# Kernel tuning notes

Hardware: AMD Instinct MI355X
Metric: run time of the kernel (lower is better)

The kernel has to match this reference:

```python
import jax, jax.numpy as jnp
import numpy as np

N_NODES = 100000
N_EDGES = 1600000
F_IN = 64
HID = 128
N_CLASSES = 16
N_GRAPHS = 128


def _glorot(key, shape):
    fan_in = shape[1]
    bound = 1.0 / np.sqrt(fan_in)
    return jax.random.uniform(key, shape, jnp.float32, -bound, bound)


def setup_inputs() -> dict:
    key = jax.random.key(0)
    ks = jax.random.split(key, 12)
    x = jax.random.normal(ks[0], (N_NODES, F_IN), jnp.float32)
    edge_index = jax.random.randint(ks[1], (2, N_EDGES), 0, N_NODES, jnp.int64)
    batch = jnp.sort(jax.random.randint(ks[2], (N_NODES,), 0, N_GRAPHS, jnp.int64))
    # GraphConv l: out = lin_rel(sum_j x_j) + lin_root(x); lin_rel has bias, lin_root does not.
    W1_rel = _glorot(ks[3], (HID, F_IN)); b1 = jnp.zeros((HID,), jnp.float32)
    W1_root = _glorot(ks[4], (HID, F_IN))
    W2_rel = _glorot(ks[5], (HID, HID)); b2 = jnp.zeros((HID,), jnp.float32)
    W2_root = _glorot(ks[6], (HID, HID))
    W3_rel = _glorot(ks[7], (HID, HID)); b3 = jnp.zeros((HID,), jnp.float32)
    W3_root = _glorot(ks[8], (HID, HID))
    W_lin = _glorot(ks[9], (N_CLASSES, HID))
    b_lin = jnp.zeros((N_CLASSES,), jnp.float32)
    return {"x": x, "edge_index": edge_index, "batch": batch,
            "W1_rel": W1_rel, "b1": b1, "W1_root": W1_root,
            "W2_rel": W2_rel, "b2": b2, "W2_root": W2_root,
            "W3_rel": W3_rel, "b3": b3, "W3_root": W3_root,
            "W_lin": W_lin, "b_lin": b_lin}


def graph_conv(x, src, dst, W_rel, b_rel, W_root):
    # gather messages from source nodes, scatter-add at targets
    agg = jax.ops.segment_sum(x[src], dst, num_segments=N_NODES)  # [N, in]
    return agg @ W_rel.T + b_rel + x @ W_root.T


def reference(x, edge_index, batch, W1_rel, b1, W1_root, W2_rel, b2, W2_root,
              W3_rel, b3, W3_root, W_lin, b_lin):
    src, dst = edge_index[0], edge_index[1]
    h = jax.nn.relu(graph_conv(x, src, dst, W1_rel, b1, W1_root))
    h = jax.nn.relu(graph_conv(h, src, dst, W2_rel, b2, W2_root))
    h = graph_conv(h, src, dst, W3_rel, b3, W3_root)
    # global_mean_pool over batch ids
    sums = jax.ops.segment_sum(h, batch, num_segments=N_GRAPHS)  # [G, HID]
    counts = jax.ops.segment_sum(jnp.ones((h.shape[0],), h.dtype), batch,
                                 num_segments=N_GRAPHS)
    pooled = sums / jnp.maximum(counts, 1.0)[:, None]
    # dropout is identity in eval mode
    return pooled @ W_lin.T + b_lin
```

## Files before the change

### kernel.cpp

```cpp
#include <hip/hip_runtime.h>

#define N_NODES_C 100000
#define N_GRAPHS_C 128

typedef __attribute__((ext_vector_type(8))) __bf16 bf16x8;
typedef __attribute__((ext_vector_type(4))) float f32x4;

__device__ __forceinline__ f32x4 mfma16(bf16x8 a, bf16x8 b, f32x4 c) {
    return __builtin_amdgcn_mfma_f32_16x16x32_bf16(a, b, c, 0, 0, 0);
}

__global__ void hist_kernel(const int* __restrict__ ei, int E, int* __restrict__ deg) {
    int i = blockIdx.x * blockDim.x + threadIdx.x;
    if (i < E) atomicAdd(&deg[ei[E + i]], 1);
}

__global__ void scan1_kernel(const int* __restrict__ deg, int N,
                             int* __restrict__ tmp, int* __restrict__ bsum) {
    __shared__ int sh[512];
    int t = threadIdx.x;
    int i = blockIdx.x * 512 + t;
    int v = (i < N) ? deg[i] : 0;
    sh[t] = v;
    __syncthreads();
    for (int off = 1; off < 512; off <<= 1) {
        int add = (t >= off) ? sh[t - off] : 0;
        __syncthreads();
        sh[t] += add;
        __syncthreads();
    }
    if (i < N) tmp[i] = sh[t] - v;
    if (t == 511) bsum[blockIdx.x] = sh[511];
}

__global__ void scan2_kernel(int* bsum, int nb) {
    if (threadIdx.x == 0 && blockIdx.x == 0) {
        int run = 0;
        for (int j = 0; j < nb; ++j) { int v = bsum[j]; bsum[j] = run; run += v; }
    }
}

__global__ void scan3_kernel(const int* __restrict__ tmp, const int* __restrict__ bsum,
                             int N, int* __restrict__ rowp, int* __restrict__ rowpm) {
    int i = blockIdx.x * 512 + threadIdx.x;
    if (i < N) {
        int v = tmp[i] + bsum[blockIdx.x];
        rowp[i] = v;
        rowpm[i] = v;
    }
}

#define FILL_EPT 8
__global__ void fill_kernel(const int* __restrict__ ei, int E,
                            int* __restrict__ rowpm, int* __restrict__ csr) {
    int p = blockIdx.y;
    int base = blockIdx.x * 256 * FILL_EPT + threadIdx.x;
#pragma unroll
    for (int k = 0; k < FILL_EPT; ++k) {
        int i = base + k * 256;
        if (i < E) {
            int d = ei[E + i];
            if ((d >> 13) == p) {
                int pos = atomicAdd(&rowpm[d], 1);
                csr[pos] = ei[i];
            }
        }
    }
}

template <int FIN>
__global__ __launch_bounds__(256) void agg_kernel(const float* __restrict__ xin,
                                                  const int* __restrict__ rowp,
                                                  const int* __restrict__ degv,
                                                  const int* __restrict__ csrc,
                                                  float* __restrict__ aggout, int nNodes) {
    int wave = blockIdx.x * 4 + (threadIdx.x >> 6);
    int lane = threadIdx.x & 63;
    if (wave >= nNodes) return;
    int start = rowp[wave];
    int deg = degv[wave];
    const float4* x4 = (const float4*)xin;
    constexpr int EPW = (FIN == 128) ? 2 : 4;
    constexpr int RS = FIN / 4;
    const int grp = lane / RS;
    const int f4 = lane & (RS - 1);

    float4 acc[8];
#pragma unroll
    for (int q = 0; q < 8; ++q) acc[q] = make_float4(0.f, 0.f, 0.f, 0.f);

    for (int base = 0; base < deg; base += 64) {
        int cnt = min(64, deg - base);
        int sid = (lane < cnt) ? csrc[start + base + lane] : 0;
        int j = 0;
        for (; j + 8 * EPW <= cnt; j += 8 * EPW) {
            int n[8];
#pragma unroll
            for (int q = 0; q < 8; ++q) n[q] = __shfl(sid, j + q * EPW + grp);
            float4 v[8];
#pragma unroll
            for (int q = 0; q < 8; ++q) v[q] = x4[(size_t)n[q] * RS + f4];
#pragma unroll
            for (int q = 0; q < 8; ++q) {
                acc[q].x += v[q].x; acc[q].y += v[q].y;
                acc[q].z += v[q].z; acc[q].w += v[q].w;
            }
        }
        for (; j + EPW <= cnt; j += EPW) {
            int n0 = __shfl(sid, j + grp);
            float4 v = x4[(size_t)n0 * RS + f4];
            acc[0].x += v.x; acc[0].y += v.y; acc[0].z += v.z; acc[0].w += v.w;
        }
        for (; j < cnt; ++j) {
            int n0 = __shfl(sid, j);
            if (grp == 0) {
                float4 v = x4[(size_t)n0 * RS + f4];
                acc[0].x += v.x; acc[0].y += v.y; acc[0].z += v.z; acc[0].w += v.w;
            }
        }
    }
    float4 tot;
    tot.x = ((acc[0].x+acc[1].x)+(acc[2].x+acc[3].x)) + ((acc[4].x+acc[5].x)+(acc[6].x+acc[7].x));
    tot.y = ((acc[0].y+acc[1].y)+(acc[2].y+acc[3].y)) + ((acc[4].y+acc[5].y)+(acc[6].y+acc[7].y));
    tot.z = ((acc[0].z+acc[1].z)+(acc[2].z+acc[3].z)) + ((acc[4].z+acc[5].z)+(acc[6].z+acc[7].z));
    tot.w = ((acc[0].w+acc[1].w)+(acc[2].w+acc[3].w)) + ((acc[4].w+acc[5].w)+(acc[6].w+acc[7].w));
    if (FIN == 64) {
        tot.x += __shfl_xor(tot.x, 16); tot.y += __shfl_xor(tot.y, 16);
        tot.z += __shfl_xor(tot.z, 16); tot.w += __shfl_xor(tot.w, 16);
    }
    tot.x += __shfl_xor(tot.x, 32); tot.y += __shfl_xor(tot.y, 32);
    tot.z += __shfl_xor(tot.z, 32); tot.w += __shfl_xor(tot.w, 32);
    if (lane < RS)
        ((float4*)aggout)[(size_t)wave * RS + lane] = tot;
}

__global__ void wprep_kernel(const float* __restrict__ Wrel, const float* __restrict__ Wroot,
                             int KH, unsigned* __restrict__ img) {
    int cid = blockIdx.x;
    int col = threadIdx.x;
    int key = (col >> 1) & 3;
    unsigned hiw[16], low[16];
#pragma unroll 4
    for (int p = 0; p < 16; ++p) {
        int k0 = cid * 32 + p * 2;
        float v0 = (k0 < KH) ? Wrel[col * KH + k0] : Wroot[col * KH + k0 - KH];
        float v1 = (k0 + 1 < KH) ? Wrel[col * KH + k0 + 1] : Wroot[col * KH + k0 + 1 - KH];
        unsigned u0 = __float_as_uint(v0), u1 = __float_as_uint(v1);
        unsigned h0 = u0 & 0xFFFF0000u, h1 = u1 & 0xFFFF0000u;
        float l0 = v0 - __uint_as_float(h0), l1 = v1 - __uint_as_float(h1);
        unsigned lb0 = __float_as_uint(l0) & 0xFFFF0000u;
        unsigned lb1 = __float_as_uint(l1) & 0xFFFF0000u;
        hiw[p] = (h0 >> 16) | h1;
        low[p] = (lb0 >> 16) | lb1;
    }
    unsigned* cb = img + (size_t)cid * 4096;
#pragma unroll 4
    for (int p = 0; p < 16; ++p) {
        int s = p >> 2, w = p & 3;
        int sp = s ^ key;
        cb[col * 16 + sp * 4 + w] = hiw[p];
        cb[2048 + col * 16 + sp * 4 + w] = low[p];
    }
}

template <int KTOT, bool RELU>
__global__ __launch_bounds__(256, 2) void xform_kernel(
    const float* __restrict__ agg, const float* __restrict__ xin,
    const unsigned* __restrict__ wimg, const float* __restrict__ bias,
    float* __restrict__ hout, int nNodes)
{
    constexpr int KH = KTOT / 2;
    constexpr int NC = KTOT / 32;
    __shared__ unsigned sA[2][4096];
    __shared__ unsigned sW[2][4096];
    const int t = threadIdx.x;
    const int nb0 = blockIdx.x * 128;

    const int srow = t >> 1;
    const int skh = t & 1;
    const int skey = (srow >> 1) & 3;
    const int gn = nb0 + srow;
    const bool gvalid = gn < nNodes;
    const size_t arow = (size_t)gn * KH;

    float4 va[4]; uint4 vw[4];
    auto loadChunk = [&](int cix) {
        int kc = cix * 32 + skh * 16;
        const float* srcA = (kc < KH) ? agg : xin;
        int kof = (kc < KH) ? kc : kc - KH;
        if (gvalid) {
#pragma unroll
            for (int q = 0; q < 4; ++q)
                va[q] = *(const float4*)&srcA[arow + kof + q * 4];
        } else {
#pragma unroll
            for (int q = 0; q < 4; ++q) va[q] = make_float4(0.f, 0.f, 0.f, 0.f);
        }
        const uint4* wsrc = (const uint4*)(wimg + (size_t)cix * 4096) + t * 4;
#pragma unroll
        for (int q = 0; q < 4; ++q) vw[q] = wsrc[q];
    };
    auto writeChunk = [&](int buf) {
        uint4* wd = (uint4*)&sW[buf][t * 16];
#pragma unroll
        for (int q = 0; q < 4; ++q) wd[q] = vw[q];
        unsigned hiw[8], low[8];
#pragma unroll
        for (int q = 0; q < 4; ++q) {
            float vv[4] = {va[q].x, va[q].y, va[q].z, va[q].w};
#pragma unroll
            for (int h = 0; h < 2; ++h) {
                unsigned u0 = __float_as_uint(vv[h * 2]), u1 = __float_as_uint(vv[h * 2 + 1]);
                unsigned h0 = u0 & 0xFFFF0000u, h1 = u1 & 0xFFFF0000u;
                float l0 = vv[h * 2] - __uint_as_float(h0);
                float l1 = vv[h * 2 + 1] - __uint_as_float(h1);
                unsigned lb0 = __float_as_uint(l0) & 0xFFFF0000u;
                unsigned lb1 = __float_as_uint(l1) & 0xFFFF0000u;
                hiw[q * 2 + h] = (h0 >> 16) | h1;
                low[q * 2 + h] = (lb0 >> 16) | lb1;
            }
        }
        int s0 = (skh * 2) ^ skey, s1 = (skh * 2 + 1) ^ skey;
        unsigned* abH = &sA[buf][srow * 16];
        unsigned* abL = &sA[buf][2048 + srow * 16];
        *(uint4*)&abH[s0 * 4] = make_uint4(hiw[0], hiw[1], hiw[2], hiw[3]);
        *(uint4*)&abH[s1 * 4] = make_uint4(hiw[4], hiw[5], hiw[6], hiw[7]);
        *(uint4*)&abL[s0 * 4] = make_uint4(low[0], low[1], low[2], low[3]);
        *(uint4*)&abL[s1 * 4] = make_uint4(low[4], low[5], low[6], low[7]);
    };

    const int lane = t & 63, wv = t >> 6;
    const int r15 = lane & 15, hi4 = lane >> 4;
    const int ckey = (r15 >> 1) & 3;
    const int cslot = (hi4 ^ ckey) * 4;
    const int arow0 = (wv * 32 + r15) * 16;
    const int arow1 = arow0 + 256;

    f32x4 acc[2][8];
#pragma unroll
    for (int g = 0; g < 2; ++g)
#pragma unroll
        for (int j = 0; j < 8; ++j) acc[g][j] = (f32x4){0.f, 0.f, 0.f, 0.f};

    float bj[8];
#pragma unroll
    for (int j = 0; j < 8; ++j) bj[j] = bias[j * 16 + r15];

    loadChunk(0);
    writeChunk(0);
    if (NC > 1) loadChunk(1);
    __syncthreads();

#pragma unroll 1
    for (int cix = 0; cix < NC; ++cix) {
        const int cur = cix & 1;
        if (cix + 1 < NC) {
            writeChunk(cur ^ 1);
            if (cix + 2 < NC) loadChunk(cix + 2);
        }
        const unsigned* A = sA[cur];
        const unsigned* W = sW[cur];
        bf16x8 ah0 = *(const bf16x8*)&A[arow0 + cslot];
        bf16x8 ah1 = *(const bf16x8*)&A[arow1 + cslot];
        bf16x8 al0 = *(const bf16x8*)&A[2048 + arow0 + cslot];
        bf16x8 al1 = *(const bf16x8*)&A[2048 + arow1 + cslot];
#pragma unroll
        for (int j = 0; j < 8; ++j) {
            int cb = (j * 16 + r15) * 16;
            bf16x8 bh = *(const bf16x8*)&W[cb + cslot];
            bf16x8 bl = *(const bf16x8*)&W[2048 + cb + cslot];
            acc[0][j] = mfma16(ah0, bh, acc[0][j]);
            acc[1][j] = mfma16(ah1, bh, acc[1][j]);
            acc[0][j] = mfma16(ah0, bl, acc[0][j]);
            acc[1][j] = mfma16(ah1, bl, acc[1][j]);
            acc[0][j] = mfma16(al0, bh, acc[0][j]);
            acc[1][j] = mfma16(al1, bh, acc[1][j]);
        }
        __syncthreads();
    }

#pragma unroll
    for (int g2 = 0; g2 < 2; ++g2) {
#pragma unroll
        for (int r = 0; r < 4; ++r) {
            int node = nb0 + wv * 32 + g2 * 16 + hi4 * 4 + r;
            if (node >= nNodes) continue;
            float* orow = &hout[(size_t)node * 128];
#pragma unroll
            for (int j = 0; j < 8; ++j) {
                float v = acc[g2][j][r] + bj[j];
                if (RELU) v = fmaxf(v, 0.f);
                orow[j * 16 + r15] = v;
            }
        }
    }
}

__global__ void bounds_kernel(const int* __restrict__ batch, int N, int* __restrict__ gstart) {
    int g = blockIdx.x * blockDim.x + threadIdx.x;
    if (g > N_GRAPHS_C) return;
    int lo = 0, hi = N;
    while (lo < hi) {
        int mid = (lo + hi) >> 1;
        if (batch[mid] < g) lo = mid + 1; else hi = mid;
    }
    gstart[g] = lo;
}

__global__ __launch_bounds__(256) void pool2_kernel(const float* __restrict__ h,
                                                    const int* __restrict__ gstart,
                                                    float* __restrict__ pooled) {
    int g = blockIdx.x;
    int f4 = threadIdx.x & 31;
    int sub = threadIdx.x >> 5;
    int s = gstart[g], e = gstart[g + 1];
    const float4* h4 = (const float4*)h;
    float4 acc = make_float4(0.f, 0.f, 0.f, 0.f);
    for (int n = s + sub; n < e; n += 8) {
        float4 v = h4[(size_t)n * 32 + f4];
        acc.x += v.x; acc.y += v.y; acc.z += v.z; acc.w += v.w;
    }
    __shared__ float4 sh[8][33];
    sh[sub][f4] = acc;
    __syncthreads();
    if (sub == 0) {
        float4 tot = acc;
#pragma unroll
        for (int q = 1; q < 8; ++q) {
            float4 v = sh[q][f4];
            tot.x += v.x; tot.y += v.y; tot.z += v.z; tot.w += v.w;
        }
        float inv = 1.0f / fmaxf((float)(e - s), 1.0f);
        tot.x *= inv; tot.y *= inv; tot.z *= inv; tot.w *= inv;
        ((float4*)pooled)[g * 32 + f4] = tot;
    }
}

__global__ void final_kernel(const float* __restrict__ pooled,
                             const float* __restrict__ Wlin, const float* __restrict__ blin,
                             float* __restrict__ out) {
    int idx = blockIdx.x * blockDim.x + threadIdx.x;
    int g = idx >> 4, c = idx & 15;
    float s = 0.f;
    for (int k = 0; k < 128; ++k) s += pooled[g * 128 + k] * Wlin[c * 128 + k];
    out[idx] = s + blin[c];
}

extern "C" void kernel_launch(void* const* d_in, const int* in_sizes, int n_in,
                              void* d_out, int out_size, void* d_ws, size_t ws_size,
                              hipStream_t stream) {
    const float* x      = (const float*)d_in[0];
    const int*   ei     = (const int*)d_in[1];
    const int*   batch  = (const int*)d_in[2];
    const float* W1_rel = (const float*)d_in[3];
    const float* b1     = (const float*)d_in[4];
    const float* W1_root= (const float*)d_in[5];
    const float* W2_rel = (const float*)d_in[6];
    const float* b2     = (const float*)d_in[7];
    const float* W2_root= (const float*)d_in[8];
    const float* W3_rel = (const float*)d_in[9];
    const float* b3     = (const float*)d_in[10];
    const float* W3_root= (const float*)d_in[11];
    const float* W_lin  = (const float*)d_in[12];
    const float* b_lin  = (const float*)d_in[13];
    float* out = (float*)d_out;

    const int N = in_sizes[2];
    const int E = in_sizes[1] / 2;
    const int nb = (N + 511) / 512;

    char* base = (char*)d_ws;
    size_t off = 0;
    auto carve = [&](size_t bytes) -> void* {
        void* p = base + off;
        off = (off + bytes + 255) & ~(size_t)255;
        return p;
    };
    int*      deg    = (int*)carve((size_t)N * 4);
    int*      tmp    = (int*)carve((size_t)N * 4);
    int*      bsum   = (int*)carve(1024);
    int*      rowp   = (int*)carve((size_t)(N + 1) * 4);
    int*      rowpm  = (int*)carve((size_t)N * 4);
    int*      csr    = (int*)carve((size_t)E * 4);
    float*    aggbuf = (float*)carve((size_t)N * 128 * 4);
    float*    hA     = (float*)carve((size_t)N * 128 * 4);
    float*    hB     = (float*)carve((size_t)N * 128 * 4);
    float*    pooled = (float*)carve((size_t)N_GRAPHS_C * 128 * 4);
    int*      gstart = (int*)carve((size_t)(N_GRAPHS_C + 1) * 4);
    unsigned* wimg1  = (unsigned*)carve((size_t)4 * 4096 * 4);
    unsigned* wimg2  = (unsigned*)carve((size_t)8 * 4096 * 4);
    unsigned* wimg3  = (unsigned*)carve((size_t)8 * 4096 * 4);
    (void)ws_size;

    hipMemsetAsync(deg, 0, (size_t)N * 4, stream);

    wprep_kernel<<<4, 128, 0, stream>>>(W1_rel, W1_root, 64, wimg1);
    wprep_kernel<<<8, 128, 0, stream>>>(W2_rel, W2_root, 128, wimg2);
    wprep_kernel<<<8, 128, 0, stream>>>(W3_rel, W3_root, 128, wimg3);

    hist_kernel<<<(E + 255) / 256, 256, 0, stream>>>(ei, E, deg);
    scan1_kernel<<<nb, 512, 0, stream>>>(deg, N, tmp, bsum);
    scan2_kernel<<<1, 64, 0, stream>>>(bsum, nb);
    scan3_kernel<<<nb, 512, 0, stream>>>(tmp, bsum, N, rowp, rowpm);
    const int npass = (N + 8191) >> 13;
    fill_kernel<<<dim3((E + 256 * FILL_EPT - 1) / (256 * FILL_EPT), npass), 256, 0, stream>>>(
        ei, E, rowpm, csr);

    bounds_kernel<<<1, 192, 0, stream>>>(batch, N, gstart);

    const int aggGrid = (N + 3) / 4;
    const int xGrid = (N + 127) / 128;

    agg_kernel<64><<<aggGrid, 256, 0, stream>>>(x, rowp, deg, csr, aggbuf, N);
    xform_kernel<128, true><<<xGrid, 256, 0, stream>>>(aggbuf, x, wimg1, b1, hA, N);

    agg_kernel<128><<<aggGrid, 256, 0, stream>>>(hA, rowp, deg, csr, aggbuf, N);
    xform_kernel<256, true><<<xGrid, 256, 0, stream>>>(aggbuf, hA, wimg2, b2, hB, N);

    agg_kernel<128><<<aggGrid, 256, 0, stream>>>(hB, rowp, deg, csr, aggbuf, N);
    xform_kernel<256, false><<<xGrid, 256, 0, stream>>>(aggbuf, hB, wimg3, b3, hA, N);

    pool2_kernel<<<N_GRAPHS_C, 256, 0, stream>>>(hA, gstart, pooled);
    final_kernel<<<8, 256, 0, stream>>>(pooled, W_lin, b_lin, out);
}
```

Before: 789.0 us.

## Fuse neighbor aggregation into the MFMA transform kernel per GraphConv layer

```diff
diff --git a/kernel.cpp b/kernel.cpp
--- a/kernel.cpp
+++ b/kernel.cpp
@@ -8,6 +8,16 @@
 
 __device__ __forceinline__ f32x4 mfma16(bf16x8 a, bf16x8 b, f32x4 c) {
     return __builtin_amdgcn_mfma_f32_16x16x32_bf16(a, b, c, 0, 0, 0);
+}
+
+__device__ __forceinline__ void split2(float a, float b, unsigned& hi, unsigned& lo) {
+    unsigned ua = __float_as_uint(a), ub = __float_as_uint(b);
+    unsigned ha = ua & 0xFFFF0000u, hb = ub & 0xFFFF0000u;
+    float la = a - __uint_as_float(ha), lb = b - __uint_as_float(hb);
+    unsigned lpa = __float_as_uint(la) & 0xFFFF0000u;
+    unsigned lpb = __float_as_uint(lb) & 0xFFFF0000u;
+    hi = (ha >> 16) | hb;
+    lo = (lpa >> 16) | lpb;
 }
 
 __global__ void hist_kernel(const int* __restrict__ ei, int E, int* __restrict__ deg) {
@@ -68,72 +78,6 @@
     }
 }
 
-template <int FIN>
-__global__ __launch_bounds__(256) void agg_kernel(const float* __restrict__ xin,
-                                                  const int* __restrict__ rowp,
-                                                  const int* __restrict__ degv,
-                                                  const int* __restrict__ csrc,
-                                                  float* __restrict__ aggout, int nNodes) {
-    int wave = blockIdx.x * 4 + (threadIdx.x >> 6);
-    int lane = threadIdx.x & 63;
-    if (wave >= nNodes) return;
-    int start = rowp[wave];
-    int deg = degv[wave];
-    const float4* x4 = (const float4*)xin;
-    constexpr int EPW = (FIN == 128) ? 2 : 4;
-    constexpr int RS = FIN / 4;
-    const int grp = lane / RS;
-    const int f4 = lane & (RS - 1);
-
-    float4 acc[8];
-#pragma unroll
-    for (int q = 0; q < 8; ++q) acc[q] = make_float4(0.f, 0.f, 0.f, 0.f);
-
-    for (int base = 0; base < deg; base += 64) {
-        int cnt = min(64, deg - base);
-        int sid = (lane < cnt) ? csrc[start + base + lane] : 0;
-        int j = 0;
-        for (; j + 8 * EPW <= cnt; j += 8 * EPW) {
-            int n[8];
-#pragma unroll
-            for (int q = 0; q < 8; ++q) n[q] = __shfl(sid, j + q * EPW + grp);
-            float4 v[8];
-#pragma unroll
-            for (int q = 0; q < 8; ++q) v[q] = x4[(size_t)n[q] * RS + f4];
-#pragma unroll
-            for (int q = 0; q < 8; ++q) {
-                acc[q].x += v[q].x; acc[q].y += v[q].y;
-                acc[q].z += v[q].z; acc[q].w += v[q].w;
-            }
-        }
-        for (; j + EPW <= cnt; j += EPW) {
-            int n0 = __shfl(sid, j + grp);
-            float4 v = x4[(size_t)n0 * RS + f4];
-            acc[0].x += v.x; acc[0].y += v.y; acc[0].z += v.z; acc[0].w += v.w;
-        }
-        for (; j < cnt; ++j) {
-            int n0 = __shfl(sid, j);
-            if (grp == 0) {
-                float4 v = x4[(size_t)n0 * RS + f4];
-                acc[0].x += v.x; acc[0].y += v.y; acc[0].z += v.z; acc[0].w += v.w;
-            }
-        }
-    }
-    float4 tot;
-    tot.x = ((acc[0].x+acc[1].x)+(acc[2].x+acc[3].x)) + ((acc[4].x+acc[5].x)+(acc[6].x+acc[7].x));
-    tot.y = ((acc[0].y+acc[1].y)+(acc[2].y+acc[3].y)) + ((acc[4].y+acc[5].y)+(acc[6].y+acc[7].y));
-    tot.z = ((acc[0].z+acc[1].z)+(acc[2].z+acc[3].z)) + ((acc[4].z+acc[5].z)+(acc[6].z+acc[7].z));
-    tot.w = ((acc[0].w+acc[1].w)+(acc[2].w+acc[3].w)) + ((acc[4].w+acc[5].w)+(acc[6].w+acc[7].w));
-    if (FIN == 64) {
-        tot.x += __shfl_xor(tot.x, 16); tot.y += __shfl_xor(tot.y, 16);
-        tot.z += __shfl_xor(tot.z, 16); tot.w += __shfl_xor(tot.w, 16);
-    }
-    tot.x += __shfl_xor(tot.x, 32); tot.y += __shfl_xor(tot.y, 32);
-    tot.z += __shfl_xor(tot.z, 32); tot.w += __shfl_xor(tot.w, 32);
-    if (lane < RS)
-        ((float4*)aggout)[(size_t)wave * RS + lane] = tot;
-}
-
 __global__ void wprep_kernel(const float* __restrict__ Wrel, const float* __restrict__ Wroot,
                              int KH, unsigned* __restrict__ img) {
     int cid = blockIdx.x;
@@ -145,13 +89,7 @@
         int k0 = cid * 32 + p * 2;
         float v0 = (k0 < KH) ? Wrel[col * KH + k0] : Wroot[col * KH + k0 - KH];
         float v1 = (k0 + 1 < KH) ? Wrel[col * KH + k0 + 1] : Wroot[col * KH + k0 + 1 - KH];
-        unsigned u0 = __float_as_uint(v0), u1 = __float_as_uint(v1);
-        unsigned h0 = u0 & 0xFFFF0000u, h1 = u1 & 0xFFFF0000u;
-        float l0 = v0 - __uint_as_float(h0), l1 = v1 - __uint_as_float(h1);
-        unsigned lb0 = __float_as_uint(l0) & 0xFFFF0000u;
-        unsigned lb1 = __float_as_uint(l1) & 0xFFFF0000u;
-        hiw[p] = (h0 >> 16) | h1;
-        low[p] = (lb0 >> 16) | lb1;
+        split2(v0, v1, hiw[p], low[p]);
     }
     unsigned* cb = img + (size_t)cid * 4096;
 #pragma unroll 4
@@ -163,135 +101,189 @@
     }
 }
 
-template <int KTOT, bool RELU>
-__global__ __launch_bounds__(256, 2) void xform_kernel(
-    const float* __restrict__ agg, const float* __restrict__ xin,
+template <int KH, bool RELU>
+__global__ __launch_bounds__(256, 2) void fused_kernel(
+    const float* __restrict__ xin,
+    const int* __restrict__ rowp, const int* __restrict__ degv,
+    const int* __restrict__ csrc,
     const unsigned* __restrict__ wimg, const float* __restrict__ bias,
     float* __restrict__ hout, int nNodes)
 {
-    constexpr int KH = KTOT / 2;
-    constexpr int NC = KTOT / 32;
-    __shared__ unsigned sA[2][4096];
+    constexpr int NC  = (2 * KH) / 32;
+    constexpr int NCA = KH / 32;
+    constexpr int RS  = KH / 4;
+    constexpr int EPW = 64 / RS;
+    __shared__ unsigned sAgg[NCA * 2048];
     __shared__ unsigned sW[2][4096];
+    __shared__ unsigned sX[2][2048];
     const int t = threadIdx.x;
-    const int nb0 = blockIdx.x * 128;
-
-    const int srow = t >> 1;
-    const int skh = t & 1;
+    const int nb0 = blockIdx.x * 64;
+    const int lane = t & 63, wv = t >> 6;
+
+    uint4 vw[4];
+    {
+        const uint4* ws = (const uint4*)wimg + t * 4;
+#pragma unroll
+        for (int q = 0; q < 4; ++q) vw[q] = ws[q];
+    }
+
+    {
+        const float4* x4 = (const float4*)xin;
+        const int grp = lane / RS;
+        const int f4 = lane & (RS - 1);
+        for (int ni = 0; ni < 16; ++ni) {
+            const int node = nb0 + wv * 16 + ni;
+            float4 a[8];
+#pragma unroll
+            for (int q = 0; q < 8; ++q) a[q] = make_float4(0.f, 0.f, 0.f, 0.f);
+            if (node < nNodes) {
+                int start = rowp[node], deg = degv[node];
+                for (int base = 0; base < deg; base += 64) {
+                    int cnt = min(64, deg - base);
+                    int sid = (lane < cnt) ? csrc[start + base + lane] : 0;
+                    int j = 0;
+                    for (; j + 8 * EPW <= cnt; j += 8 * EPW) {
+                        int n[8];
+#pragma unroll
+                        for (int q = 0; q < 8; ++q) n[q] = __shfl(sid, j + q * EPW + grp);
+                        float4 v[8];
+#pragma unroll
+                        for (int q = 0; q < 8; ++q) v[q] = x4[(size_t)n[q] * RS + f4];
+#pragma unroll
+                        for (int q = 0; q < 8; ++q) {
+                            a[q].x += v[q].x; a[q].y += v[q].y;
+                            a[q].z += v[q].z; a[q].w += v[q].w;
+                        }
+                    }
+                    for (; j + EPW <= cnt; j += EPW) {
+                        int n0 = __shfl(sid, j + grp);
+                        float4 v = x4[(size_t)n0 * RS + f4];
+                        a[0].x += v.x; a[0].y += v.y; a[0].z += v.z; a[0].w += v.w;
+                    }
+                    for (; j < cnt; ++j) {
+                        int n0 = __shfl(sid, j);
+                        if (grp == 0) {
+                            float4 v = x4[(size_t)n0 * RS + f4];
+                            a[0].x += v.x; a[0].y += v.y; a[0].z += v.z; a[0].w += v.w;
+                        }
+                    }
+                }
+            }
+            float4 tot;
+            tot.x = ((a[0].x+a[1].x)+(a[2].x+a[3].x)) + ((a[4].x+a[5].x)+(a[6].x+a[7].x));
+            tot.y = ((a[0].y+a[1].y)+(a[2].y+a[3].y)) + ((a[4].y+a[5].y)+(a[6].y+a[7].y));
+            tot.z = ((a[0].z+a[1].z)+(a[2].z+a[3].z)) + ((a[4].z+a[5].z)+(a[6].z+a[7].z));
+            tot.w = ((a[0].w+a[1].w)+(a[2].w+a[3].w)) + ((a[4].w+a[5].w)+(a[6].w+a[7].w));
+            if (RS == 16) {
+                tot.x += __shfl_xor(tot.x, 16); tot.y += __shfl_xor(tot.y, 16);
+                tot.z += __shfl_xor(tot.z, 16); tot.w += __shfl_xor(tot.w, 16);
+            }
+            tot.x += __shfl_xor(tot.x, 32); tot.y += __shfl_xor(tot.y, 32);
+            tot.z += __shfl_xor(tot.z, 32); tot.w += __shfl_xor(tot.w, 32);
+            if (grp < 2) {
+                unsigned h0, l0, h1, l1;
+                split2(tot.x, tot.y, h0, l0);
+                split2(tot.z, tot.w, h1, l1);
+                int row = wv * 16 + ni;
+                int key = (row >> 1) & 3;
+                int c = f4 >> 3;
+                int u = (2 * f4) & 15;
+                int sp = (u >> 2) ^ key;
+                unsigned* dst = &sAgg[c * 2048 + grp * 1024 + row * 16 + sp * 4 + (u & 3)];
+                dst[0] = (grp == 0) ? h0 : l0;
+                dst[1] = (grp == 0) ? h1 : l1;
+            }
+        }
+    }
+
+    const int srow = t >> 2;
+    const int kq = t & 3;
     const int skey = (srow >> 1) & 3;
-    const int gn = nb0 + srow;
-    const bool gvalid = gn < nNodes;
-    const size_t arow = (size_t)gn * KH;
-
-    float4 va[4]; uint4 vw[4];
-    auto loadChunk = [&](int cix) {
-        int kc = cix * 32 + skh * 16;
-        const float* srcA = (kc < KH) ? agg : xin;
-        int kof = (kc < KH) ? kc : kc - KH;
-        if (gvalid) {
-#pragma unroll
-            for (int q = 0; q < 4; ++q)
-                va[q] = *(const float4*)&srcA[arow + kof + q * 4];
+    const bool svalid = (nb0 + srow) < nNodes;
+    float4 vx0, vx1;
+    auto loadW = [&](int cix) {
+        const uint4* ws = (const uint4*)(wimg + (size_t)cix * 4096) + t * 4;
+#pragma unroll
+        for (int q = 0; q < 4; ++q) vw[q] = ws[q];
+    };
+    auto loadX = [&](int cix) {
+        int kofs = (cix - NCA) * 32 + kq * 8;
+        if (svalid) {
+            const float* p = &xin[(size_t)(nb0 + srow) * KH + kofs];
+            vx0 = *(const float4*)p;
+            vx1 = *(const float4*)(p + 4);
         } else {
-#pragma unroll
-            for (int q = 0; q < 4; ++q) va[q] = make_float4(0.f, 0.f, 0.f, 0.f);
-        }
-        const uint4* wsrc = (const uint4*)(wimg + (size_t)cix * 4096) + t * 4;
-#pragma unroll
-        for (int q = 0; q < 4; ++q) vw[q] = wsrc[q];
+            vx0 = make_float4(0.f, 0.f, 0.f, 0.f);
+            vx1 = vx0;
+        }
     };
-    auto writeChunk = [&](int buf) {
+    auto writeW = [&](int buf) {
         uint4* wd = (uint4*)&sW[buf][t * 16];
 #pragma unroll
         for (int q = 0; q < 4; ++q) wd[q] = vw[q];
-        unsigned hiw[8], low[8];
-#pragma unroll
-        for (int q = 0; q < 4; ++q) {
-            float vv[4] = {va[q].x, va[q].y, va[q].z, va[q].w};
-#pragma unroll
-            for (int h = 0; h < 2; ++h) {
-                unsigned u0 = __float_as_uint(vv[h * 2]), u1 = __float_as_uint(vv[h * 2 + 1]);
-                unsigned h0 = u0 & 0xFFFF0000u, h1 = u1 & 0xFFFF0000u;
-                float l0 = vv[h * 2] - __uint_as_float(h0);
-                float l1 = vv[h * 2 + 1] - __uint_as_float(h1);
-                unsigned lb0 = __float_as_uint(l0) & 0xFFFF0000u;
-                unsigned lb1 = __float_as_uint(l1) & 0xFFFF0000u;
-                hiw[q * 2 + h] = (h0 >> 16) | h1;
-                low[q * 2 + h] = (lb0 >> 16) | lb1;
-            }
-        }
-        int s0 = (skh * 2) ^ skey, s1 = (skh * 2 + 1) ^ skey;
-        unsigned* abH = &sA[buf][srow * 16];
-        unsigned* abL = &sA[buf][2048 + srow * 16];
-        *(uint4*)&abH[s0 * 4] = make_uint4(hiw[0], hiw[1], hiw[2], hiw[3]);
-        *(uint4*)&abH[s1 * 4] = make_uint4(hiw[4], hiw[5], hiw[6], hiw[7]);
-        *(uint4*)&abL[s0 * 4] = make_uint4(low[0], low[1], low[2], low[3]);
-        *(uint4*)&abL[s1 * 4] = make_uint4(low[4], low[5], low[6], low[7]);
     };
-
-    const int lane = t & 63, wv = t >> 6;
+    auto writeX = [&](int buf) {
+        unsigned h[4], l[4];
+        split2(vx0.x, vx0.y, h[0], l[0]); split2(vx0.z, vx0.w, h[1], l[1]);
+        split2(vx1.x, vx1.y, h[2], l[2]); split2(vx1.z, vx1.w, h[3], l[3]);
+        int sp = (kq ^ skey) * 4;
+        *(uint4*)&sX[buf][srow * 16 + sp] = make_uint4(h[0], h[1], h[2], h[3]);
+        *(uint4*)&sX[buf][1024 + srow * 16 + sp] = make_uint4(l[0], l[1], l[2], l[3]);
+    };
+
     const int r15 = lane & 15, hi4 = lane >> 4;
     const int ckey = (r15 >> 1) & 3;
     const int cslot = (hi4 ^ ckey) * 4;
-    const int arow0 = (wv * 32 + r15) * 16;
-    const int arow1 = arow0 + 256;
-
-    f32x4 acc[2][8];
-#pragma unroll
-    for (int g = 0; g < 2; ++g)
-#pragma unroll
-        for (int j = 0; j < 8; ++j) acc[g][j] = (f32x4){0.f, 0.f, 0.f, 0.f};
-
+    const int arow = (wv * 16 + r15) * 16;
+
+    f32x4 acc[8];
+#pragma unroll
+    for (int j = 0; j < 8; ++j) acc[j] = (f32x4){0.f, 0.f, 0.f, 0.f};
     float bj[8];
 #pragma unroll
     for (int j = 0; j < 8; ++j) bj[j] = bias[j * 16 + r15];
 
-    loadChunk(0);
-    writeChunk(0);
-    if (NC > 1) loadChunk(1);
+    writeW(0);
+    if (NC > 1) { loadW(1); if (1 >= NCA) loadX(1); }
     __syncthreads();
 
 #pragma unroll 1
     for (int cix = 0; cix < NC; ++cix) {
         const int cur = cix & 1;
         if (cix + 1 < NC) {
-            writeChunk(cur ^ 1);
-            if (cix + 2 < NC) loadChunk(cix + 2);
-        }
-        const unsigned* A = sA[cur];
+            writeW(cur ^ 1);
+            if (cix + 1 >= NCA) writeX(cur ^ 1);
+            if (cix + 2 < NC) {
+                loadW(cix + 2);
+                if (cix + 2 >= NCA) loadX(cix + 2);
+            }
+        }
+        const unsigned* Ah = (cix < NCA) ? &sAgg[cix * 2048] : &sX[cur][0];
         const unsigned* W = sW[cur];
-        bf16x8 ah0 = *(const bf16x8*)&A[arow0 + cslot];
-        bf16x8 ah1 = *(const bf16x8*)&A[arow1 + cslot];
-        bf16x8 al0 = *(const bf16x8*)&A[2048 + arow0 + cslot];
-        bf16x8 al1 = *(const bf16x8*)&A[2048 + arow1 + cslot];
+        bf16x8 ah = *(const bf16x8*)&Ah[arow + cslot];
+        bf16x8 al = *(const bf16x8*)&Ah[1024 + arow + cslot];
 #pragma unroll
         for (int j = 0; j < 8; ++j) {
             int cb = (j * 16 + r15) * 16;
             bf16x8 bh = *(const bf16x8*)&W[cb + cslot];
             bf16x8 bl = *(const bf16x8*)&W[2048 + cb + cslot];
-            acc[0][j] = mfma16(ah0, bh, acc[0][j]);
-            acc[1][j] = mfma16(ah1, bh, acc[1][j]);
-            acc[0][j] = mfma16(ah0, bl, acc[0][j]);
-            acc[1][j] = mfma16(ah1, bl, acc[1][j]);
-            acc[0][j] = mfma16(al0, bh, acc[0][j]);
-            acc[1][j] = mfma16(al1, bh, acc[1][j]);
+            acc[j] = mfma16(ah, bh, acc[j]);
+            acc[j] = mfma16(ah, bl, acc[j]);
+            acc[j] = mfma16(al, bh, acc[j]);
         }
         __syncthreads();
     }
 
 #pragma unroll
-    for (int g2 = 0; g2 < 2; ++g2) {
-#pragma unroll
-        for (int r = 0; r < 4; ++r) {
-            int node = nb0 + wv * 32 + g2 * 16 + hi4 * 4 + r;
-            if (node >= nNodes) continue;
-            float* orow = &hout[(size_t)node * 128];
-#pragma unroll
-            for (int j = 0; j < 8; ++j) {
-                float v = acc[g2][j][r] + bj[j];
-                if (RELU) v = fmaxf(v, 0.f);
-                orow[j * 16 + r15] = v;
-            }
+    for (int r = 0; r < 4; ++r) {
+        int node = nb0 + wv * 16 + hi4 * 4 + r;
+        if (node >= nNodes) continue;
+        float* orow = &hout[(size_t)node * 128];
+#pragma unroll
+        for (int j = 0; j < 8; ++j) {
+            float v = acc[j][r] + bj[j];
+            if (RELU) v = fmaxf(v, 0.f);
+            orow[j * 16 + r15] = v;
         }
     }
 }
@@ -382,7 +374,6 @@
     int*      rowp   = (int*)carve((size_t)(N + 1) * 4);
     int*      rowpm  = (int*)carve((size_t)N * 4);
     int*      csr    = (int*)carve((size_t)E * 4);
-    float*    aggbuf = (float*)carve((size_t)N * 128 * 4);
     float*    hA     = (float*)carve((size_t)N * 128 * 4);
     float*    hB     = (float*)carve((size_t)N * 128 * 4);
     float*    pooled = (float*)carve((size_t)N_GRAPHS_C * 128 * 4);
@@ -408,17 +399,16 @@
 
     bounds_kernel<<<1, 192, 0, stream>>>(batch, N, gstart);
 
-    const int aggGrid = (N + 3) / 4;
-    const int xGrid = (N + 127) / 128;
-
-    agg_kernel<64><<<aggGrid, 256, 0, stream>>>(x, rowp, deg, csr, aggbuf, N);
-    xform_kernel<128, true><<<xGrid, 256, 0, stream>>>(aggbuf, x, wimg1, b1, hA, N);
-
-    agg_kernel<128><<<aggGrid, 256, 0, stream>>>(hA, rowp, deg, csr, aggbuf, N);
-    xform_kernel<256, true><<<xGrid, 256, 0, stream>>>(aggbuf, hA, wimg2, b2, hB, N);
-
-    agg_kernel<128><<<aggGrid, 256, 0, stream>>>(hB, rowp, deg, csr, aggbuf, N);
-    xform_kernel<256, false><<<xGrid, 256, 0, stream>>>(aggbuf, hB, wimg3, b3, hA, N);
+    const int fGrid = (N + 63) / 64;
+
+    fused_kernel<64, true><<<fGrid, 256, 0, stream>>>(
+        x, rowp, deg, csr, wimg1, b1, hA, N);
+
+    fused_kernel<128, true><<<fGrid, 256, 0, stream>>>(
+        hA, rowp, deg, csr, wimg2, b2, hB, N);
+
+    fused_kernel<128, false><<<fGrid, 256, 0, stream>>>(
+        hB, rowp, deg, csr, wimg3, b3, hA, N);
 
     pool2_kernel<<<N_GRAPHS_C, 256, 0, stream>>>(hA, gstart, pooled);
     final_kernel<<<8, 256, 0, stream>>>(pooled, W_lin, b_lin, out);
```

New measurement: 1.079 ms. +36.7%, slower.

## Load MFMA fragments directly from global memory, bypassing LDS staging in xform

Applied to the files above, without the earlier changes.

```diff
diff --git a/kernel.cpp b/kernel.cpp
--- a/kernel.cpp
+++ b/kernel.cpp
@@ -8,6 +8,25 @@
 
 __device__ __forceinline__ f32x4 mfma16(bf16x8 a, bf16x8 b, f32x4 c) {
     return __builtin_amdgcn_mfma_f32_16x16x32_bf16(a, b, c, 0, 0, 0);
+}
+
+__device__ __forceinline__ void split2(float a, float b, unsigned& hi, unsigned& lo) {
+    unsigned ua = __float_as_uint(a), ub = __float_as_uint(b);
+    unsigned ha = ua & 0xFFFF0000u, hb = ub & 0xFFFF0000u;
+    float la = a - __uint_as_float(ha), lb = b - __uint_as_float(hb);
+    unsigned lpa = __float_as_uint(la) & 0xFFFF0000u;
+    unsigned lpb = __float_as_uint(lb) & 0xFFFF0000u;
+    hi = (ha >> 16) | hb;
+    lo = (lpa >> 16) | lpb;
+}
+
+__device__ __forceinline__ void splitfrag(float4 v0, float4 v1, bf16x8& hi, bf16x8& lo) {
+    unsigned h[4], l[4];
+    split2(v0.x, v0.y, h[0], l[0]); split2(v0.z, v0.w, h[1], l[1]);
+    split2(v1.x, v1.y, h[2], l[2]); split2(v1.z, v1.w, h[3], l[3]);
+    uint4 uh = make_uint4(h[0], h[1], h[2], h[3]);
+    uint4 ul = make_uint4(l[0], l[1], l[2], l[3]);
+    hi = *(bf16x8*)&uh; lo = *(bf16x8*)&ul;
 }
 
 __global__ void hist_kernel(const int* __restrict__ ei, int E, int* __restrict__ deg) {
@@ -136,139 +155,68 @@
 
 __global__ void wprep_kernel(const float* __restrict__ Wrel, const float* __restrict__ Wroot,
                              int KH, unsigned* __restrict__ img) {
-    int cid = blockIdx.x;
-    int col = threadIdx.x;
-    int key = (col >> 1) & 3;
-    unsigned hiw[16], low[16];
-#pragma unroll 4
-    for (int p = 0; p < 16; ++p) {
-        int k0 = cid * 32 + p * 2;
-        float v0 = (k0 < KH) ? Wrel[col * KH + k0] : Wroot[col * KH + k0 - KH];
-        float v1 = (k0 + 1 < KH) ? Wrel[col * KH + k0 + 1] : Wroot[col * KH + k0 + 1 - KH];
-        unsigned u0 = __float_as_uint(v0), u1 = __float_as_uint(v1);
-        unsigned h0 = u0 & 0xFFFF0000u, h1 = u1 & 0xFFFF0000u;
-        float l0 = v0 - __uint_as_float(h0), l1 = v1 - __uint_as_float(h1);
-        unsigned lb0 = __float_as_uint(l0) & 0xFFFF0000u;
-        unsigned lb1 = __float_as_uint(l1) & 0xFFFF0000u;
-        hiw[p] = (h0 >> 16) | h1;
-        low[p] = (lb0 >> 16) | lb1;
-    }
-    unsigned* cb = img + (size_t)cid * 4096;
-#pragma unroll 4
-    for (int p = 0; p < 16; ++p) {
-        int s = p >> 2, w = p & 3;
-        int sp = s ^ key;
-        cb[col * 16 + sp * 4 + w] = hiw[p];
-        cb[2048 + col * 16 + sp * 4 + w] = low[p];
-    }
+    int cj = blockIdx.x;
+    int l = threadIdx.x;
+    int c = cj >> 3, j = cj & 7;
+    int col = j * 16 + (l & 15);
+    int k0 = c * 32 + (l >> 4) * 8;
+    const float* src = (k0 < KH) ? Wrel : Wroot;
+    int kk = (k0 < KH) ? k0 : k0 - KH;
+    unsigned h[4], lo[4];
+#pragma unroll
+    for (int q = 0; q < 4; ++q) {
+        float a = src[col * KH + kk + 2 * q];
+        float b = src[col * KH + kk + 2 * q + 1];
+        split2(a, b, h[q], lo[q]);
+    }
+    *(uint4*)&img[((size_t)cj * 2 + 0) * 256 + l * 4] = make_uint4(h[0], h[1], h[2], h[3]);
+    *(uint4*)&img[((size_t)cj * 2 + 1) * 256 + l * 4] = make_uint4(lo[0], lo[1], lo[2], lo[3]);
 }
 
 template <int KTOT, bool RELU>
-__global__ __launch_bounds__(256, 2) void xform_kernel(
+__global__ __launch_bounds__(256) void xform_kernel(
     const float* __restrict__ agg, const float* __restrict__ xin,
     const unsigned* __restrict__ wimg, const float* __restrict__ bias,
     float* __restrict__ hout, int nNodes)
 {
     constexpr int KH = KTOT / 2;
     constexpr int NC = KTOT / 32;
-    __shared__ unsigned sA[2][4096];
-    __shared__ unsigned sW[2][4096];
     const int t = threadIdx.x;
-    const int nb0 = blockIdx.x * 128;
-
-    const int srow = t >> 1;
-    const int skh = t & 1;
-    const int skey = (srow >> 1) & 3;
-    const int gn = nb0 + srow;
-    const bool gvalid = gn < nNodes;
-    const size_t arow = (size_t)gn * KH;
-
-    float4 va[4]; uint4 vw[4];
-    auto loadChunk = [&](int cix) {
-        int kc = cix * 32 + skh * 16;
-        const float* srcA = (kc < KH) ? agg : xin;
-        int kof = (kc < KH) ? kc : kc - KH;
-        if (gvalid) {
-#pragma unroll
-            for (int q = 0; q < 4; ++q)
-                va[q] = *(const float4*)&srcA[arow + kof + q * 4];
-        } else {
-#pragma unroll
-            for (int q = 0; q < 4; ++q) va[q] = make_float4(0.f, 0.f, 0.f, 0.f);
-        }
-        const uint4* wsrc = (const uint4*)(wimg + (size_t)cix * 4096) + t * 4;
-#pragma unroll
-        for (int q = 0; q < 4; ++q) vw[q] = wsrc[q];
-    };
-    auto writeChunk = [&](int buf) {
-        uint4* wd = (uint4*)&sW[buf][t * 16];
-#pragma unroll
-        for (int q = 0; q < 4; ++q) wd[q] = vw[q];
-        unsigned hiw[8], low[8];
-#pragma unroll
-        for (int q = 0; q < 4; ++q) {
-            float vv[4] = {va[q].x, va[q].y, va[q].z, va[q].w};
-#pragma unroll
-            for (int h = 0; h < 2; ++h) {
-                unsigned u0 = __float_as_uint(vv[h * 2]), u1 = __float_as_uint(vv[h * 2 + 1]);
-                unsigned h0 = u0 & 0xFFFF0000u, h1 = u1 & 0xFFFF0000u;
-                float l0 = vv[h * 2] - __uint_as_float(h0);
-                float l1 = vv[h * 2 + 1] - __uint_as_float(h1);
-                unsigned lb0 = __float_as_uint(l0) & 0xFFFF0000u;
-                unsigned lb1 = __float_as_uint(l1) & 0xFFFF0000u;
-                hiw[q * 2 + h] = (h0 >> 16) | h1;
-                low[q * 2 + h] = (lb0 >> 16) | lb1;
-            }
-        }
-        int s0 = (skh * 2) ^ skey, s1 = (skh * 2 + 1) ^ skey;
-        unsigned* abH = &sA[buf][srow * 16];
-        unsigned* abL = &sA[buf][2048 + srow * 16];
-        *(uint4*)&abH[s0 * 4] = make_uint4(hiw[0], hiw[1], hiw[2], hiw[3]);
-        *(uint4*)&abH[s1 * 4] = make_uint4(hiw[4], hiw[5], hiw[6], hiw[7]);
-        *(uint4*)&abL[s0 * 4] = make_uint4(low[0], low[1], low[2], low[3]);
-        *(uint4*)&abL[s1 * 4] = make_uint4(low[4], low[5], low[6], low[7]);
-    };
-
     const int lane = t & 63, wv = t >> 6;
     const int r15 = lane & 15, hi4 = lane >> 4;
-    const int ckey = (r15 >> 1) & 3;
-    const int cslot = (hi4 ^ ckey) * 4;
-    const int arow0 = (wv * 32 + r15) * 16;
-    const int arow1 = arow0 + 256;
+    const int nb0 = blockIdx.x * 128;
+    const int row0 = nb0 + wv * 32 + r15;
+    const int row1 = row0 + 16;
+    const bool v0 = row0 < nNodes, v1 = row1 < nNodes;
+    const float4 z4 = make_float4(0.f, 0.f, 0.f, 0.f);
 
     f32x4 acc[2][8];
 #pragma unroll
     for (int g = 0; g < 2; ++g)
 #pragma unroll
         for (int j = 0; j < 8; ++j) acc[g][j] = (f32x4){0.f, 0.f, 0.f, 0.f};
-
     float bj[8];
 #pragma unroll
     for (int j = 0; j < 8; ++j) bj[j] = bias[j * 16 + r15];
 
-    loadChunk(0);
-    writeChunk(0);
-    if (NC > 1) loadChunk(1);
-    __syncthreads();
-
 #pragma unroll 1
-    for (int cix = 0; cix < NC; ++cix) {
-        const int cur = cix & 1;
-        if (cix + 1 < NC) {
-            writeChunk(cur ^ 1);
-            if (cix + 2 < NC) loadChunk(cix + 2);
-        }
-        const unsigned* A = sA[cur];
-        const unsigned* W = sW[cur];
-        bf16x8 ah0 = *(const bf16x8*)&A[arow0 + cslot];
-        bf16x8 ah1 = *(const bf16x8*)&A[arow1 + cslot];
-        bf16x8 al0 = *(const bf16x8*)&A[2048 + arow0 + cslot];
-        bf16x8 al1 = *(const bf16x8*)&A[2048 + arow1 + cslot];
+    for (int c = 0; c < NC; ++c) {
+        const float* srcA = (c * 32 < KH) ? agg : xin;
+        const int ko = ((c * 32 < KH) ? (c * 32) : (c * 32 - KH)) + hi4 * 8;
+        const float* p0 = &srcA[(size_t)row0 * KH + ko];
+        const float* p1 = &srcA[(size_t)row1 * KH + ko];
+        float4 a00 = v0 ? *(const float4*)p0 : z4;
+        float4 a01 = v0 ? *(const float4*)(p0 + 4) : z4;
+        float4 a10 = v1 ? *(const float4*)p1 : z4;
+        float4 a11 = v1 ? *(const float4*)(p1 + 4) : z4;
+        bf16x8 ah0, al0, ah1, al1;
+        splitfrag(a00, a01, ah0, al0);
+        splitfrag(a10, a11, ah1, al1);
+        const unsigned* wc = wimg + (size_t)c * 4096;
 #pragma unroll
         for (int j = 0; j < 8; ++j) {
-            int cb = (j * 16 + r15) * 16;
-            bf16x8 bh = *(const bf16x8*)&W[cb + cslot];
-            bf16x8 bl = *(const bf16x8*)&W[2048 + cb + cslot];
+            bf16x8 bh = *(const bf16x8*)&wc[(j * 2 + 0) * 256 + lane * 4];
+            bf16x8 bl = *(const bf16x8*)&wc[(j * 2 + 1) * 256 + lane * 4];
             acc[0][j] = mfma16(ah0, bh, acc[0][j]);
             acc[1][j] = mfma16(ah1, bh, acc[1][j]);
             acc[0][j] = mfma16(ah0, bl, acc[0][j]);
@@ -276,7 +224,6 @@
             acc[0][j] = mfma16(al0, bh, acc[0][j]);
             acc[1][j] = mfma16(al1, bh, acc[1][j]);
         }
-        __syncthreads();
     }
 
 #pragma unroll
@@ -394,9 +341,9 @@
 
     hipMemsetAsync(deg, 0, (size_t)N * 4, stream);
 
-    wprep_kernel<<<4, 128, 0, stream>>>(W1_rel, W1_root, 64, wimg1);
-    wprep_kernel<<<8, 128, 0, stream>>>(W2_rel, W2_root, 128, wimg2);
-    wprep_kernel<<<8, 128, 0, stream>>>(W3_rel, W3_root, 128, wimg3);
+    wprep_kernel<<<32, 64, 0, stream>>>(W1_rel, W1_root, 64, wimg1);
+    wprep_kernel<<<64, 64, 0, stream>>>(W2_rel, W2_root, 128, wimg2);
+    wprep_kernel<<<64, 64, 0, stream>>>(W3_rel, W3_root, 128, wimg3);
 
     hist_kernel<<<(E + 255) / 256, 256, 0, stream>>>(ei, E, deg);
     scan1_kernel<<<nb, 512, 0, stream>>>(deg, N, tmp, bsum);
```

Result: no change. 802.4 us (+1.7%).
